# Kernel tuning notes

Hardware: AMD Instinct MI355X
Metric: run time of the kernel (lower is better)

Reference implementation:

```python
import jax, jax.numpy as jnp
import numpy as np

NUM_HEADS = 16
DIM = 1024
B, L = 2, 2048
NEG = -10000000000.0


def setup_inputs() -> dict:
    key = jax.random.key(0)
    ks = jax.random.split(key, 8)
    queries = jax.random.normal(ks[0], (B, L, DIM), dtype=jnp.float32)
    keys = jax.random.normal(ks[1], (B, L, DIM), dtype=jnp.float32)
    values = jax.random.normal(ks[2], (B, L, DIM), dtype=jnp.float32)
    mask = jax.random.uniform(ks[3], (B, L, L)) < 0.1
    s = 1.0 / np.sqrt(DIM)
    Wq = jax.random.uniform(ks[4], (DIM, DIM), minval=-s, maxval=s, dtype=jnp.float32)
    Wk = jax.random.uniform(ks[5], (DIM, DIM), minval=-s, maxval=s, dtype=jnp.float32)
    Wv = jax.random.uniform(ks[6], (DIM, DIM), minval=-s, maxval=s, dtype=jnp.float32)
    Wo = jax.random.uniform(ks[7], (DIM, DIM), minval=-s, maxval=s, dtype=jnp.float32)
    return {"queries": queries, "keys": keys, "values": values, "mask": mask,
            "Wq": Wq, "Wk": Wk, "Wv": Wv, "Wo": Wo}


def reference(queries, keys, values, mask, Wq, Wk, Wv, Wo):
    b, l, d = queries.shape
    h = NUM_HEADS
    dk = d // h
    # torch Linear(bias=False): y = x @ W.T ; then view(b, l, dk, h) -> head axis LAST
    qs = (queries @ Wq.T).reshape(b, l, dk, h)
    ks = (keys @ Wk.T).reshape(b, l, dk, h)
    vs = (values @ Wv.T).reshape(b, l, dk, h)
    # routing is None in the live code path
    w = jnp.einsum('bidh,bodh->bioh', qs, ks) / jnp.sqrt(jnp.asarray(dk, jnp.float32))
    w = jnp.where(mask[..., None], NEG, w)          # masked_fill where mask True
    w = jax.nn.softmax(w, axis=-2)                   # softmax over key axis 'o'
    mha = jnp.einsum('bioh,bodh->bidh', w, vs).reshape(b, l, d)
    # dropout is identity in eval mode
    return mha @ Wo.T
```

## Files before the change

### kernel.cpp

```cpp
#include <hip/hip_runtime.h>
#include <hip/hip_bf16.h>
#include <cstdint>
#include <cstddef>

typedef unsigned short ushort_t;
typedef __attribute__((ext_vector_type(8))) short short8;
typedef __attribute__((ext_vector_type(8))) unsigned short ushort8;
typedef __attribute__((ext_vector_type(4))) unsigned short ushort4v;
typedef __attribute__((ext_vector_type(4))) float f32x4;
typedef __attribute__((ext_vector_type(2))) unsigned long long ull2;
typedef __attribute__((ext_vector_type(2))) unsigned int uint2v;

#define LPAD 72

#define PIPE_WAIT_BAR(N) do {                                              \
    asm volatile("s_waitcnt vmcnt(" #N ") lgkmcnt(0)" ::: "memory");       \
    __builtin_amdgcn_s_barrier();                                          \
    asm volatile("" ::: "memory");                                         \
} while (0)

__device__ __forceinline__ unsigned short f2bf(float f) {
    unsigned int x = __float_as_uint(f);
    unsigned int r = x + 0x7fffu + ((x >> 16) & 1u);
    return (unsigned short)(r >> 16);
}

__device__ __forceinline__ unsigned int cvt_pk_bf16(float lo, float hi) {
    unsigned int r;
    asm("v_cvt_pk_bf16_f32 %0, %1, %2" : "=v"(r) : "v"(lo), "v"(hi));
    return r;
}

__device__ __forceinline__ void async16(const ushort_t* g, ushort_t* l) {
    __builtin_amdgcn_global_load_lds(
        (const __attribute__((address_space(1))) unsigned int*)g,
        (__attribute__((address_space(3))) unsigned int*)l,
        16, 0, 0);
}

__global__ __launch_bounds__(256) void prep1(const float* __restrict__ q,
                                             const float* __restrict__ k,
                                             const float* __restrict__ v,
                                             const float* __restrict__ Wq,
                                             const float* __restrict__ Wk,
                                             const float* __restrict__ Wv,
                                             ushort_t* __restrict__ qb,
                                             ushort_t* __restrict__ kb,
                                             ushort_t* __restrict__ vb,
                                             ushort_t* __restrict__ Wqb,
                                             ushort_t* __restrict__ Wkb,
                                             ushort_t* __restrict__ Wvb) {
    const int bid = blockIdx.x;
    const int tid = threadIdx.x;
    const float* src; ushort_t* dst; float sc = 1.0f;
    if (bid < 6144) {
        const int z   = bid >> 11;
        const int blk = bid & 2047;
        const size_t idx = (((size_t)blk << 8) + tid) << 3;
        src = ((z == 0) ? q : (z == 1) ? k : v) + idx;
        dst = ((z == 0) ? qb : (z == 1) ? kb : vb) + idx;
        if (z == 0) sc = 0.125f;
    } else {
        const int qq   = bid - 6144;
        const int wsel = qq >> 9;
        const size_t idx = (((size_t)(qq & 511) << 8) + tid) << 3;
        src = ((wsel == 0) ? Wq : (wsel == 1) ? Wk : Wv) + idx;
        dst = ((wsel == 0) ? Wqb : (wsel == 1) ? Wkb : Wvb) + idx;
    }
    f32x4 a0 = *(const f32x4*)src, a1 = *(const f32x4*)(src + 4);
    ushort8 o;
    #pragma unroll
    for (int j = 0; j < 4; j++) { o[j] = f2bf(a0[j] * sc); o[j + 4] = f2bf(a1[j] * sc); }
    *(ushort8*)dst = o;
}

__global__ __launch_bounds__(256) void prep2(const int* __restrict__ mask,
                                             const float* __restrict__ Wo,
                                             ushort_t* __restrict__ WoH,
                                             unsigned long long* __restrict__ Mbits) {
    __shared__ float srow[1024 + 64];
    const int bid = blockIdx.x;
    const int tid = threadIdx.x;
    if (bid < 4096) {
        const int row  = bid;
        const int w    = tid >> 6;
        const int lane = tid & 63;
        const int* mrow = mask + (size_t)row * 2048;
        #pragma unroll
        for (int it = 0; it < 8; it++) {
            const int o = (it << 8) + (w << 6) + lane;
            const unsigned long long bb = __ballot(mrow[o] != 0);
            if (lane == 0) Mbits[(size_t)((it << 2) + w) * 4096 + row] = bb;
        }
    } else {
        const int j = bid - 4096;
        f32x4 v = *(const f32x4*)(Wo + (size_t)j * 1024 + (tid << 2));
        #pragma unroll
        for (int s = 0; s < 4; s++) { const int c = (tid << 2) + s; srow[c + (c >> 4)] = v[s]; }
        __syncthreads();
        #pragma unroll
        for (int s = 0; s < 4; s++) {
            const int k = tid + (s << 8);
            const int col = ((k & 63) << 4) + (k >> 6);
            WoH[(size_t)j * 1024 + k] = f2bf(srow[col + (col >> 4)]);
        }
    }
}

__global__ __launch_bounds__(512, 2) void gemm_proj(const ushort_t* __restrict__ qb,
                                                    const ushort_t* __restrict__ kb,
                                                    const ushort_t* __restrict__ vb,
                                                    const ushort_t* __restrict__ Wqb,
                                                    const ushort_t* __restrict__ Wkb,
                                                    const ushort_t* __restrict__ Wvb,
                                                    ushort_t* __restrict__ Qh,
                                                    ushort_t* __restrict__ Kh,
                                                    ushort_t* __restrict__ VhT) {
    __shared__ ushort_t Xs[3][8192];
    __shared__ ushort_t Ws[3][8192];

    const int lid  = blockIdx.x;
    const int nIdx = lid / 48;
    const int rem  = lid % 48;
    const int z    = rem >> 4;
    const int mIdx = rem & 15;
    const int n0   = nIdx << 8;
    const int m0   = mIdx << 8;

    const ushort_t* Xb = (z == 0) ? qb : (z == 1) ? kb : vb;
    const ushort_t* Wb = (z == 0) ? Wqb : (z == 1) ? Wkb : Wvb;

    const int tid  = threadIdx.x;
    const int w    = tid >> 6;
    const int lane = tid & 63;
    const int lm   = lane & 15;
    const int quad = lane >> 4;
    const int wm   = w & 1;
    const int wn   = w >> 1;

    f32x4 acc[8][4];
    #pragma unroll
    for (int i = 0; i < 8; i++)
        #pragma unroll
        for (int j = 0; j < 4; j++) acc[i][j] = (f32x4){0.f, 0.f, 0.f, 0.f};

    auto stage = [&](int k0, int buf) {
        #pragma unroll
        for (int i = 0; i < 2; i++) {
            const int L   = (((w << 1) + i) << 6) + lane;
            const int c4  = L >> 8, row = L & 255;
            const int lb  = (((w << 1) + i) << 6) << 3;
            async16(Xb + (size_t)(m0 + row) * 1024 + k0 + (c4 << 3), &Xs[buf][lb]);
            async16(Wb + (size_t)(n0 + row) * 1024 + k0 + (c4 << 3), &Ws[buf][lb]);
        }
    };

    stage(0, 0);
    stage(32, 1);
    PIPE_WAIT_BAR(4);

    int cur = 0;
    for (int t = 0; t < 32; ++t) {
        int nb = cur + 2; if (nb >= 3) nb -= 3;
        if (t < 30) stage((t + 2) << 5, nb);
        short8 af[8], bf4[4];
        #pragma unroll
        for (int mf = 0; mf < 8; mf++)
            af[mf] = *(const short8*)&Xs[cur][((quad << 8) + (wm << 7) + (mf << 4) + lm) << 3];
        #pragma unroll
        for (int nf = 0; nf < 4; nf++)
            bf4[nf] = *(const short8*)&Ws[cur][((quad << 8) + (wn << 6) + (nf << 4) + lm) << 3];
        #pragma unroll
        for (int mf = 0; mf < 8; mf++)
            #pragma unroll
            for (int nf = 0; nf < 4; nf++)
                acc[mf][nf] = __builtin_amdgcn_mfma_f32_16x16x32_bf16(af[mf], bf4[nf], acc[mf][nf], 0, 0, 0);
        if (t < 30)       PIPE_WAIT_BAR(4);
        else if (t == 30) PIPE_WAIT_BAR(0);
        cur += 1; if (cur == 3) cur = 0;
    }

    const int bb    = m0 >> 11;
    const int l0    = m0 & 2047;
    const int dbase = (n0 >> 4) + (wn << 2);
    if (z != 2) {
        ushort_t* OUT = (z == 0) ? Qh : Kh;
        #pragma unroll
        for (int mf = 0; mf < 8; mf++)
            #pragma unroll
            for (int r = 0; r < 4; r++) {
                const int row = (wm << 7) + (mf << 4) + (quad << 2) + r;
                ushort4v o = { f2bf(acc[mf][0][r]), f2bf(acc[mf][1][r]),
                               f2bf(acc[mf][2][r]), f2bf(acc[mf][3][r]) };
                *(ushort4v*)(OUT + ((size_t)((bb << 4) + lm) * 2048 + l0 + row) * 64 + dbase) = o;
            }
    } else {
        #pragma unroll
        for (int mf = 0; mf < 8; mf++)
            #pragma unroll
            for (int nf = 0; nf < 4; nf++) {
                const int lbase = l0 + (wm << 7) + (mf << 4) + (quad << 2);
                ushort4v o = { f2bf(acc[mf][nf][0]), f2bf(acc[mf][nf][1]),
                               f2bf(acc[mf][nf][2]), f2bf(acc[mf][nf][3]) };
                *(ushort4v*)(VhT + ((size_t)((bb << 4) + lm) * 64 + dbase + nf) * 2048 + lbase) = o;
            }
    }
}

__global__ __launch_bounds__(256) void gemm_out(const ushort_t* __restrict__ mhaH,
                                                const ushort_t* __restrict__ WoH,
                                                float* __restrict__ C) {
    __shared__ ushort_t Xs[3][4096];
    __shared__ ushort_t Ws[3][2048];

    const int lid  = blockIdx.x;
    const int mIdx = ((lid & 7) << 2) | ((lid >> 3) & 3);
    const int nIdx = lid >> 5;
    const int m0   = mIdx << 7;
    const int n0   = nIdx << 6;

    const int tid  = threadIdx.x;
    const int w    = tid >> 6;
    const int lane = tid & 63;
    const int lm   = lane & 15;
    const int quad = lane >> 4;
    const int wm   = w & 1;
    const int wn   = w >> 1;
    const int ab   = m0 >> 11;
    const int al0  = m0 & 2047;

    f32x4 acc[4][2];
    #pragma unroll
    for (int i = 0; i < 4; i++)
        #pragma unroll
        for (int j = 0; j < 2; j++) acc[i][j] = (f32x4){0.f, 0.f, 0.f, 0.f};

    auto stage = [&](int k0, int buf) {
        const int h  = k0 >> 6;
        const int d0 = k0 & 63;
        #pragma unroll
        for (int i = 0; i < 2; i++) {
            const int L   = (i << 8) + (w << 6) + lane;
            const int c4  = L >> 7, row = L & 127;
            async16(mhaH + ((size_t)(ab * 16 + h) * 2048 + al0 + row) * 64 + d0 + (c4 << 3),
                    &Xs[buf][((i << 8) + (w << 6)) << 3]);
        }
        {
            const int L   = (w << 6) + lane;
            const int c4  = L >> 6, row = L & 63;
            async16(WoH + (size_t)(n0 + row) * 1024 + k0 + (c4 << 3),
                    &Ws[buf][(w << 6) << 3]);
        }
    };

    stage(0, 0);
    stage(32, 1);
    PIPE_WAIT_BAR(3);

    int cur = 0;
    for (int t = 0; t < 32; ++t) {
        int nb = cur + 2; if (nb >= 3) nb -= 3;
        if (t < 30) stage((t + 2) << 5, nb);
        short8 af[4], bf2[2];
        #pragma unroll
        for (int mf = 0; mf < 4; mf++)
            af[mf] = *(const short8*)&Xs[cur][((quad << 7) + (wm << 6) + (mf << 4) + lm) << 3];
        #pragma unroll
        for (int nf = 0; nf < 2; nf++)
            bf2[nf] = *(const short8*)&Ws[cur][((quad << 6) + (wn << 5) + (nf << 4) + lm) << 3];
        #pragma unroll
        for (int mf = 0; mf < 4; mf++)
            #pragma unroll
            for (int nf = 0; nf < 2; nf++)
                acc[mf][nf] = __builtin_amdgcn_mfma_f32_16x16x32_bf16(af[mf], bf2[nf], acc[mf][nf], 0, 0, 0);
        if (t < 30)       PIPE_WAIT_BAR(3);
        else if (t == 30) PIPE_WAIT_BAR(0);
        cur += 1; if (cur == 3) cur = 0;
    }
    #pragma unroll
    for (int mf = 0; mf < 4; mf++)
        #pragma unroll
        for (int nf = 0; nf < 2; nf++)
            #pragma unroll
            for (int r = 0; r < 4; r++) {
                const int row = m0 + (wm << 6) + (mf << 4) + (quad << 2) + r;
                const int col = n0 + (wn << 5) + (nf << 4) + lm;
                C[(size_t)row * 1024 + col] = acc[mf][nf][r];
            }
}

__global__ __launch_bounds__(256, 2) void flash_attn(const ushort_t* __restrict__ Qh,
                                                     const ushort_t* __restrict__ Kh,
                                                     const ushort_t* __restrict__ VhT,
                                                     const unsigned long long* __restrict__ Mbits,
                                                     ushort_t* __restrict__ mhaH) {
    __shared__ ushort_t Ks[3][4096];
    __shared__ ushort_t Vs[3][4096];
    __shared__ ushort_t Pw[4][2][16 * LPAD];

    const int tid  = threadIdx.x;
    const int w    = tid >> 6;
    const int lane = tid & 63;
    const int lm   = lane & 15;
    const int quad = lane >> 4;
    const int lid  = blockIdx.x;
    const int bh   = ((lid & 7) << 2) | ((lid >> 3) & 3);
    const int q0   = (lid >> 5) << 7;
    const int b    = bh >> 4;

    const ushort_t* Qb  = Qh  + ((size_t)bh << 17);
    const ushort_t* Kb  = Kh  + ((size_t)bh << 17);
    const ushort_t* Vtb = VhT + ((size_t)bh << 17);

    short8 aq[2][2];
    #pragma unroll
    for (int g = 0; g < 2; g++) {
        const ushort_t* qp = Qb + (size_t)(q0 + (w << 5) + (g << 4) + lm) * 64 + (quad << 3);
        aq[g][0] = *(const short8*)qp;
        aq[g][1] = *(const short8*)(qp + 32);
    }

    float l_part[2][4] = {{0.f,0.f,0.f,0.f},{0.f,0.f,0.f,0.f}};
    f32x4 o_acc[2][4] = {{{0.f,0.f,0.f,0.f},{0.f,0.f,0.f,0.f},{0.f,0.f,0.f,0.f},{0.f,0.f,0.f,0.f}},
                         {{0.f,0.f,0.f,0.f},{0.f,0.f,0.f,0.f},{0.f,0.f,0.f,0.f},{0.f,0.f,0.f,0.f}}};

    const int rowbase  = (b << 11) + q0 + (w << 5);
    const int shamt    = (lm & 7) << 2;
    const bool hi_half = lm >= 8;

    const ushort_t* ksrc = Kb  + (size_t)((lm << 2) + w) * 64 + (quad << 3);
    const ushort_t* vsrc = Vtb + (size_t)((w << 4) + lm) * 2048 + (quad << 3);

    auto stageKV = [&](int kt0, int buf) {
        async16(ksrc + (size_t)kt0 * 64,      &Ks[buf][((w << 7)     ) << 3]);
        async16(ksrc + (size_t)kt0 * 64 + 32, &Ks[buf][((w << 7) + 64) << 3]);
        async16(vsrc + kt0,      &Vs[buf][((w << 7)     ) << 3]);
        async16(vsrc + kt0 + 32, &Vs[buf][((w << 7) + 64) << 3]);
    };

    stageKV(0, 0);
    stageKV(64, 1);
    PIPE_WAIT_BAR(4);

    int cur = 0;
    for (int t = 0; t < 32; ++t) {
        const int kt0 = t << 6;
        int nb = cur + 2; if (nb >= 3) nb -= 3;

        const unsigned long long* Mt = Mbits + (size_t)(kt0 >> 6) * 4096 + rowbase;
        unsigned long long mb[2][4];
        #pragma unroll
        for (int g = 0; g < 2; g++) {
            const unsigned long long* mp = Mt + (g << 4) + (quad << 2);
            ull2 t0 = *(const ull2*)mp;
            ull2 t1 = *(const ull2*)(mp + 2);
            mb[g][0] = t0[0]; mb[g][1] = t0[1]; mb[g][2] = t1[0]; mb[g][3] = t1[1];
        }

        if (t < 30) stageKV(kt0 + 128, nb);

        short8 bk[4][2], bv[4][2];
        #pragma unroll
        for (int c = 0; c < 4; c++) {
            bk[c][0] = *(const short8*)&Ks[cur][((c << 7) + lane) << 3];
            bk[c][1] = *(const short8*)&Ks[cur][((c << 7) + 64 + lane) << 3];
            bv[c][0] = *(const short8*)&Vs[cur][((c << 7) + lane) << 3];
            bv[c][1] = *(const short8*)&Vs[cur][((c << 7) + 64 + lane) << 3];
        }

        f32x4 s[2][4];
        __builtin_amdgcn_s_setprio(1);
        #pragma unroll
        for (int g = 0; g < 2; g++)
            #pragma unroll
            for (int c = 0; c < 4; c++) {
                f32x4 zz = {0.f, 0.f, 0.f, 0.f};
                zz = __builtin_amdgcn_mfma_f32_16x16x32_bf16(aq[g][0], bk[c][0], zz, 0, 0, 0);
                zz = __builtin_amdgcn_mfma_f32_16x16x32_bf16(aq[g][1], bk[c][1], zz, 0, 0, 0);
                s[g][c] = zz;
            }
        __builtin_amdgcn_s_setprio(0);

        #pragma unroll
        for (int g = 0; g < 2; g++) {
            #pragma unroll
            for (int r = 0; r < 4; r++) {
                const unsigned long long m64 = mb[g][r];
                const unsigned word = hi_half ? (unsigned)(m64 >> 32) : (unsigned)m64;
                const unsigned nib  = (word >> shamt) & 0xFu;
                float p0 = __expf(s[g][0][r]); if (nib & 1u) p0 = 0.f;
                float p1 = __expf(s[g][1][r]); if (nib & 2u) p1 = 0.f;
                float p2 = __expf(s[g][2][r]); if (nib & 4u) p2 = 0.f;
                float p3 = __expf(s[g][3][r]); if (nib & 8u) p3 = 0.f;
                l_part[g][r] += (p0 + p1) + (p2 + p3);
                uint2v pv2;
                pv2[0] = cvt_pk_bf16(p0, p1);
                pv2[1] = cvt_pk_bf16(p2, p3);
                *(uint2v*)&Pw[w][g][((quad << 2) + r) * LPAD + (lm << 2)] = pv2;
            }
        }

        __builtin_amdgcn_s_setprio(1);
        #pragma unroll
        for (int g = 0; g < 2; g++) {
            short8 ap0 = *(const short8*)&Pw[w][g][lm * LPAD + (quad << 3)];
            short8 ap1 = *(const short8*)&Pw[w][g][lm * LPAD + 32 + (quad << 3)];
            #pragma unroll
            for (int cd = 0; cd < 4; cd++) {
                o_acc[g][cd] = __builtin_amdgcn_mfma_f32_16x16x32_bf16(ap0, bv[cd][0], o_acc[g][cd], 0, 0, 0);
                o_acc[g][cd] = __builtin_amdgcn_mfma_f32_16x16x32_bf16(ap1, bv[cd][1], o_acc[g][cd], 0, 0, 0);
            }
        }
        __builtin_amdgcn_s_setprio(0);

        if (t < 30)       PIPE_WAIT_BAR(4);
        else if (t == 30) PIPE_WAIT_BAR(0);
        cur += 1; if (cur == 3) cur = 0;
    }

    #pragma unroll
    for (int g = 0; g < 2; g++) {
        #pragma unroll
        for (int r = 0; r < 4; r++) {
            float l = l_part[g][r];
            l += __shfl_xor(l, 1, 64);
            l += __shfl_xor(l, 2, 64);
            l += __shfl_xor(l, 4, 64);
            l += __shfl_xor(l, 8, 64);
            const float inv_l = 1.0f / l;
            const int i = q0 + (w << 5) + (g << 4) + (quad << 2) + r;
            ushort_t* orow = mhaH + (((size_t)bh * 2048 + i) << 6);
            #pragma unroll
            for (int cd = 0; cd < 4; cd++)
                orow[(cd << 4) + lm] = f2bf(o_acc[g][cd][r] * inv_l);
        }
    }
}

extern "C" void kernel_launch(void* const* d_in, const int* in_sizes, int n_in,
                              void* d_out, int out_size, void* d_ws, size_t ws_size,
                              hipStream_t stream) {
    const float* q    = (const float*)d_in[0];
    const float* k    = (const float*)d_in[1];
    const float* v    = (const float*)d_in[2];
    const int*   mask = (const int*)d_in[3];
    const float* Wq   = (const float*)d_in[4];
    const float* Wk   = (const float*)d_in[5];
    const float* Wv   = (const float*)d_in[6];
    const float* Wo   = (const float*)d_in[7];
    float* out = (float*)d_out;

    ushort_t* qb   = (ushort_t*)d_ws;
    ushort_t* kb   = qb  + 4194304;
    ushort_t* vb   = kb  + 4194304;
    ushort_t* Wqb  = vb  + 4194304;
    ushort_t* Wkb  = Wqb + 1048576;
    ushort_t* Wvb  = Wkb + 1048576;
    ushort_t* Qh   = Wvb + 1048576;
    ushort_t* Kh   = Qh  + 4194304;
    ushort_t* VhT  = Kh  + 4194304;
    ushort_t* mhaH = qb;
    ushort_t* WoH  = kb;
    unsigned long long* Mbits = (unsigned long long*)(kb + 1048576);

    dim3 gb(256);
    prep1<<<dim3(7680), gb, 0, stream>>>(q, k, v, Wq, Wk, Wv, qb, kb, vb, Wqb, Wkb, Wvb);
    gemm_proj<<<dim3(192), dim3(512), 0, stream>>>(qb, kb, vb, Wqb, Wkb, Wvb, Qh, Kh, VhT);
    prep2<<<dim3(5120), gb, 0, stream>>>(mask, Wo, WoH, Mbits);
    flash_attn<<<dim3(512), gb, 0, stream>>>(Qh, Kh, VhT, Mbits, mhaH);
    gemm_out<<<dim3(512), gb, 0, stream>>>(mhaH, WoH, out);
}
```

Before: 303.8 us.

## Interleave QKV projection GEMM prefetch with MFMA phases using barriers and setprio

Splits each k-step of the QKV projection GEMM into four MFMA phases. The async global-to-LDS prefetch loads for the next tile are spread across those phases, and fragments are loaded incrementally, which lowers register pressure. Intra-step barriers and s_setprio raise wave priority around MFMA clusters so waves stay in lockstep and memory issue overlaps compute. The extra barriers may add sync overhead and reduce the latency hiding that free-running waves provided.

Measured after the change: 292.9 us. 1.04x faster.

```diff
diff --git a/kernel.cpp b/kernel.cpp
--- a/kernel.cpp
+++ b/kernel.cpp
@@ -144,15 +144,21 @@
         #pragma unroll
         for (int j = 0; j < 4; j++) acc[i][j] = (f32x4){0.f, 0.f, 0.f, 0.f};
 
+    auto stageX1 = [&](int k0, int buf, int i) {
+        const int L   = (((w << 1) + i) << 6) + lane;
+        const int c4  = L >> 8, row = L & 255;
+        const int lb  = (((w << 1) + i) << 6) << 3;
+        async16(Xb + (size_t)(m0 + row) * 1024 + k0 + (c4 << 3), &Xs[buf][lb]);
+    };
+    auto stageW1 = [&](int k0, int buf, int i) {
+        const int L   = (((w << 1) + i) << 6) + lane;
+        const int c4  = L >> 8, row = L & 255;
+        const int lb  = (((w << 1) + i) << 6) << 3;
+        async16(Wb + (size_t)(n0 + row) * 1024 + k0 + (c4 << 3), &Ws[buf][lb]);
+    };
     auto stage = [&](int k0, int buf) {
-        #pragma unroll
-        for (int i = 0; i < 2; i++) {
-            const int L   = (((w << 1) + i) << 6) + lane;
-            const int c4  = L >> 8, row = L & 255;
-            const int lb  = (((w << 1) + i) << 6) << 3;
-            async16(Xb + (size_t)(m0 + row) * 1024 + k0 + (c4 << 3), &Xs[buf][lb]);
-            async16(Wb + (size_t)(n0 + row) * 1024 + k0 + (c4 << 3), &Ws[buf][lb]);
-        }
+        stageX1(k0, buf, 0); stageX1(k0, buf, 1);
+        stageW1(k0, buf, 0); stageW1(k0, buf, 1);
     };
 
     stage(0, 0);
@@ -162,19 +168,61 @@
     int cur = 0;
     for (int t = 0; t < 32; ++t) {
         int nb = cur + 2; if (nb >= 3) nb -= 3;
-        if (t < 30) stage((t + 2) << 5, nb);
-        short8 af[8], bf4[4];
-        #pragma unroll
-        for (int mf = 0; mf < 8; mf++)
+        const bool pf  = (t < 30);
+        const int  k0n = (t + 2) << 5;
+        short8 af[4], bf[4];
+
+        #pragma unroll
+        for (int mf = 0; mf < 4; mf++)
             af[mf] = *(const short8*)&Xs[cur][((quad << 8) + (wm << 7) + (mf << 4) + lm) << 3];
-        #pragma unroll
-        for (int nf = 0; nf < 4; nf++)
-            bf4[nf] = *(const short8*)&Ws[cur][((quad << 8) + (wn << 6) + (nf << 4) + lm) << 3];
-        #pragma unroll
-        for (int mf = 0; mf < 8; mf++)
-            #pragma unroll
-            for (int nf = 0; nf < 4; nf++)
-                acc[mf][nf] = __builtin_amdgcn_mfma_f32_16x16x32_bf16(af[mf], bf4[nf], acc[mf][nf], 0, 0, 0);
+        bf[0] = *(const short8*)&Ws[cur][((quad << 8) + (wn << 6) + (0 << 4) + lm) << 3];
+        bf[1] = *(const short8*)&Ws[cur][((quad << 8) + (wn << 6) + (1 << 4) + lm) << 3];
+        if (pf) stageX1(k0n, nb, 0);
+        __builtin_amdgcn_s_barrier();
+        __builtin_amdgcn_s_setprio(1);
+        #pragma unroll
+        for (int mf = 0; mf < 4; mf++) {
+            acc[mf][0] = __builtin_amdgcn_mfma_f32_16x16x32_bf16(af[mf], bf[0], acc[mf][0], 0, 0, 0);
+            acc[mf][1] = __builtin_amdgcn_mfma_f32_16x16x32_bf16(af[mf], bf[1], acc[mf][1], 0, 0, 0);
+        }
+        __builtin_amdgcn_s_setprio(0);
+        __builtin_amdgcn_s_barrier();
+
+        bf[2] = *(const short8*)&Ws[cur][((quad << 8) + (wn << 6) + (2 << 4) + lm) << 3];
+        bf[3] = *(const short8*)&Ws[cur][((quad << 8) + (wn << 6) + (3 << 4) + lm) << 3];
+        if (pf) stageX1(k0n, nb, 1);
+        __builtin_amdgcn_s_barrier();
+        __builtin_amdgcn_s_setprio(1);
+        #pragma unroll
+        for (int mf = 0; mf < 4; mf++) {
+            acc[mf][2] = __builtin_amdgcn_mfma_f32_16x16x32_bf16(af[mf], bf[2], acc[mf][2], 0, 0, 0);
+            acc[mf][3] = __builtin_amdgcn_mfma_f32_16x16x32_bf16(af[mf], bf[3], acc[mf][3], 0, 0, 0);
+        }
+        __builtin_amdgcn_s_setprio(0);
+        __builtin_amdgcn_s_barrier();
+
+        #pragma unroll
+        for (int mf = 0; mf < 4; mf++)
+            af[mf] = *(const short8*)&Xs[cur][((quad << 8) + (wm << 7) + 64 + (mf << 4) + lm) << 3];
+        if (pf) stageW1(k0n, nb, 0);
+        __builtin_amdgcn_s_barrier();
+        __builtin_amdgcn_s_setprio(1);
+        #pragma unroll
+        for (int mf = 0; mf < 4; mf++) {
+            acc[4 + mf][0] = __builtin_amdgcn_mfma_f32_16x16x32_bf16(af[mf], bf[0], acc[4 + mf][0], 0, 0, 0);
+            acc[4 + mf][1] = __builtin_amdgcn_mfma_f32_16x16x32_bf16(af[mf], bf[1], acc[4 + mf][1], 0, 0, 0);
+        }
+        __builtin_amdgcn_s_setprio(0);
+        __builtin_amdgcn_s_barrier();
+
+        if (pf) stageW1(k0n, nb, 1);
+        __builtin_amdgcn_s_setprio(1);
+        #pragma unroll
+        for (int mf = 0; mf < 4; mf++) {
+            acc[4 + mf][2] = __builtin_amdgcn_mfma_f32_16x16x32_bf16(af[mf], bf[2], acc[4 + mf][2], 0, 0, 0);
+            acc[4 + mf][3] = __builtin_amdgcn_mfma_f32_16x16x32_bf16(af[mf], bf[3], acc[4 + mf][3], 0, 0, 0);
+        }
+        __builtin_amdgcn_s_setprio(0);
         if (t < 30)       PIPE_WAIT_BAR(4);
         else if (t == 30) PIPE_WAIT_BAR(0);
         cur += 1; if (cur == 3) cur = 0;
```
